# Performance work log

Measured on AMD Instinct MI355X. Metric: run time of the kernel, lower is better.

The kernel has to match this reference:

```python
import jax, jax.numpy as jnp
import numpy as np

jax.config.update("jax_enable_x64", True)

L_MAX = 9  # matches init_kwargs; K = (L_MAX+1)**2 = 100 modes
SQRT_2_OVER_PI = float(np.sqrt(2.0 / np.pi))


def _l_array(l_max):
    # l repeated 2l+1 times (one entry per (l, m) mode), as float like torch.Tensor
    ls = np.concatenate([np.full(2 * i + 1, i) for i in range(l_max + 1)])
    return jnp.asarray(ls, dtype=jnp.float64)


def _bessel_up(r, k, l_arr, l_max):
    x = r.astype(jnp.float64)[..., None] * k.astype(jnp.float64)  # [N, K]
    j0 = jnp.sin(x) / x
    y = jnp.where(l_arr == 0, j0, 0.0)
    j1 = j0 / x - jnp.cos(x) / x
    y = jnp.where(l_arr == 1, j1, y)
    for i in range(1, l_max):  # small static loop over l (l_max-1 iters)
        j2 = (2 * i + 1) / x * j1 - j0
        y = jnp.where(l_arr == i + 1, j2, y)
        j0, j1 = j1, j2
    y = jnp.where(jnp.abs(x) < 1e-30, 0.0, y)
    y = y * SQRT_2_OVER_PI * k.astype(jnp.float64)
    return y.astype(jnp.float32)


def _bessel_down(r, k, l_arr, l_max):
    x = r.astype(jnp.float64)[..., None] * k.astype(jnp.float64)  # [N, K]
    y = jnp.zeros_like(x)
    lstart = l_max + int(np.sqrt(10 * l_max))
    j2 = jnp.zeros_like(x)
    j1 = jnp.ones_like(x)
    j0 = j1
    for i in range(lstart, 0, -1):  # small static downward recurrence
        j0 = (2 * i + 1) / x * j1 - j2
        if i - 1 < l_max + 1:
            y = jnp.where(l_arr == (i - 1), j0, y)
        j2, j1 = j1, j0
    true_j0 = jnp.sinc(x / jnp.pi)  # = sin(x)/x, matches torch.sinc(r/pi)
    y = y / j0 * true_j0
    small = x < 1e-20
    y = jnp.where(small & (l_arr > 0), 0.0, y)
    y = jnp.where(small & (l_arr == 0), 1.0, y)
    y = y * SQRT_2_OVER_PI * k.astype(jnp.float64)
    return y.astype(jnp.float32)


def setup_inputs() -> dict:
    key = jax.random.key(0)
    k1, k2 = jax.random.split(key)
    N = 262144
    K = (L_MAX + 1) ** 2  # 100
    r = jax.random.uniform(k1, (N,), dtype=jnp.float32, minval=0.1, maxval=20.0)
    k = jax.random.uniform(k2, (K,), dtype=jnp.float32, minval=0.5, maxval=5.0)
    return {"r": r, "k": k}


def reference(r, k):
    l_arr = _l_array(L_MAX)
    up = _bessel_up(r, k, l_arr, L_MAX)    # [N, K] f32
    dn = _bessel_down(r, k, l_arr, L_MAX)  # [N, K] f32
    x32 = r[..., None] * k                 # f32, like the torch forward
    return jnp.where(x32 < l_arr.astype(jnp.float32), dn, up)
```

## Files before the change

kernel.cpp:

```cpp
#include <hip/hip_runtime.h>
#include <math.h>


static constexpr int KMODES  = 100;
static constexpr int NTILE   = 64;
static constexpr int LSTRIDE = 102;
static constexpr double PI_D   = 3.14159265358979323846;
static constexpr double BETA_D = 1.0 / (2.0 * PI_D);
static constexpr double S2PI_D = 0.79788456080286535588;

__device__ __forceinline__ float rcpf(float x) { return __builtin_amdgcn_rcpf(x); }
__device__ __forceinline__ float sin_rev(float a) { float r; asm("v_sin_f32 %0, %1" : "=v"(r) : "v"(a)); return r; }
__device__ __forceinline__ float cos_rev(float a) { float r; asm("v_cos_f32 %0, %1" : "=v"(r) : "v"(a)); return r; }

template<int L> struct ZC;
template<> struct ZC<2>{ static constexpr double sg[2]={3,-1};                              static constexpr double gm[1]={-3}; };
template<> struct ZC<3>{ static constexpr double sg[2]={15,-6};                             static constexpr double gm[2]={-15,1}; };
template<> struct ZC<4>{ static constexpr double sg[3]={105,-45,1};                         static constexpr double gm[2]={-105,10}; };
template<> struct ZC<5>{ static constexpr double sg[3]={945,-420,15};                       static constexpr double gm[3]={-945,105,-1}; };
template<> struct ZC<6>{ static constexpr double sg[4]={10395,-4725,210,-1};                static constexpr double gm[3]={-10395,1260,-21}; };
template<> struct ZC<7>{ static constexpr double sg[4]={135135,-62370,3150,-28};            static constexpr double gm[4]={-135135,17325,-378,1}; };
template<> struct ZC<8>{ static constexpr double sg[5]={2027025,-945945,51975,-630,1};      static constexpr double gm[4]={-2027025,270270,-6930,36}; };
template<> struct ZC<9>{ static constexpr double sg[5]={34459425,-16216200,945945,-13860,45}; static constexpr double gm[5]={-34459425,4729725,-135135,990,-1}; };

template<int L> struct WC {
  static constexpr int NS = L / 2 + 1, NG = (L + 1) / 2;
  float sg[NS], gm[NG], xc;
  constexpr WC() : sg{}, gm{}, xc(0.f) {
    constexpr double XT[10] = {0,0,0.088,0.29,0.61,1.01,1.48,2.00,2.55,3.14};
    for (int i = 0; i < NS; ++i) {
      int deg = NS - 1 - i, e = (L & 1) ? (2*deg + 2) : (2*deg + 1);
      double s = S2PI_D; for (int t = 0; t < e; ++t) s *= BETA_D;
      sg[i] = (float)(s * ZC<L>::sg[i]);
    }
    for (int i = 0; i < NG; ++i) {
      int deg = NG - 1 - i, e = (L & 1) ? (2*deg + 1) : (2*deg + 2);
      double s = S2PI_D; for (int t = 0; t < e; ++t) s *= BETA_D;
      gm[i] = (float)(s * ZC<L>::gm[i]);
    }
    xc = (float)(XT[L] * BETA_D);
  }
};

template<int N>
__device__ __forceinline__ float polyH(float y, const float (&a)[N]) {
  float h = a[0];
#pragma unroll
  for (int i = 1; i < N; ++i) h = fmaf(h, y, a[i]);
  return h;
}

template<int L>
__device__ __forceinline__ void do_l(float rv, const float2* __restrict__ ktab,
                                     float* ldsrow) {
#pragma unroll
  for (int m = 0; m < 2 * L + 1; ++m) {
    const int KK = L * L + m;
    float2 kp = ktab[KK];
    float arg = rv * kp.x;
    float res;
    if constexpr (L == 0) {
      float w = rcpf(arg);
      float s = sin_rev(arg);
      res = (s * (float)(S2PI_D * BETA_D)) * (kp.y * w);
    } else if constexpr (L == 1) {
      float w = rcpf(arg);
      float s = sin_rev(arg), c = cos_rev(arg);
      float t = c * (float)(S2PI_D * BETA_D);
      float inner = fmaf(s * w, (float)(S2PI_D * BETA_D * BETA_D), -t);
      res = (kp.y * w) * inner;
    } else {
      constexpr WC<L> wc{};
      float argc = fmaxf(arg, wc.xc);
      float w = rcpf(argc);
      float s = sin_rev(argc), c = cos_rev(argc);
      float y = w * w;
      float sgv = polyH(y, wc.sg);
      float gmv = polyH(y, wc.gm);
      float inner;
      if constexpr (L & 1) inner = fmaf(s * w, sgv, c * gmv);
      else                 inner = fmaf(c * w, gmv, s * sgv);
      res = (kp.y * w) * inner;
    }
    ldsrow[KK] = res;
  }
}

__global__ __launch_bounds__(256) void sbf_kernel(const float* __restrict__ r,
                                                  const float* __restrict__ kvec,
                                                  float* __restrict__ out) {
  __shared__ float2 ktab[KMODES];
  __shared__ float lds[NTILE * LSTRIDE];
  const int tid = threadIdx.x;
  const int w = tid >> 6, lane = tid & 63;
  const int n0 = blockIdx.x * NTILE;
  if (tid < KMODES) {
    float kv = kvec[tid];
    ktab[tid] = make_float2(kv * (float)BETA_D, kv);
  }
  float rv = r[n0 + lane];
  float* ldsrow = &lds[lane * LSTRIDE];
  __syncthreads();
  if (w == 0)      { do_l<9>(rv, ktab, ldsrow); do_l<2>(rv, ktab, ldsrow); }
  else if (w == 1) { do_l<8>(rv, ktab, ldsrow); do_l<3>(rv, ktab, ldsrow); }
  else if (w == 2) { do_l<7>(rv, ktab, ldsrow); do_l<4>(rv, ktab, ldsrow); do_l<0>(rv, ktab, ldsrow); }
  else             { do_l<6>(rv, ktab, ldsrow); do_l<5>(rv, ktab, ldsrow); do_l<1>(rv, ktab, ldsrow); }
  __syncthreads();
  unsigned e0 = (unsigned)tid * 4u;
  int row = (int)(e0 / 100u);
  int col = (int)e0 - row * 100;
  int wi  = row * LSTRIDE + col;
  float* gout = out + (size_t)n0 * KMODES + e0;
#pragma unroll
  for (int it = 0; it < 6; ++it) {
    float2 lo = *reinterpret_cast<const float2*>(&lds[wi]);
    float2 hi = *reinterpret_cast<const float2*>(&lds[wi + 2]);
    *reinterpret_cast<float4*>(gout + it * 1024) = make_float4(lo.x, lo.y, hi.x, hi.y);
    col += 24; wi += 1044;
    if (col >= 100) { col -= 100; wi += 2; }
  }
  if (tid < 64) {
    float2 lo = *reinterpret_cast<const float2*>(&lds[wi]);
    float2 hi = *reinterpret_cast<const float2*>(&lds[wi + 2]);
    *reinterpret_cast<float4*>(gout + 6 * 1024) = make_float4(lo.x, lo.y, hi.x, hi.y);
  }
}

extern "C" void kernel_launch(void* const* d_in, const int* in_sizes, int n_in,
                              void* d_out, int out_size, void* d_ws, size_t ws_size,
                              hipStream_t stream) {
  const float* r = (const float*)d_in[0];
  const float* k = (const float*)d_in[1];
  float* out = (float*)d_out;
  int N = in_sizes[0];
  int blocks = N / NTILE;
  sbf_kernel<<<blocks, 256, 0, stream>>>(r, k, out);
}
```

Baseline: 24.78 us.

## Process four tiles per block with double-buffered LDS and interleaved output flushing

Each block now handles four 64-point tiles and writes them into two alternating LDS buffers. The global stores of the previous tile are spread through the compute loop of the next tile via a Flusher that runs after every third mode. The aim is to overlap output writes with transcendental compute and to drop the per-block ktab setup, since k is read directly from global (scalar) memory and r is pre-scaled by 1/(2π). The unpadded LDS stride may add bank conflicts on the per-lane row writes. There are also 4x fewer blocks, which lowers occupancy and parallelism across the GPU.

```diff
diff --git a/kernel.cpp b/kernel.cpp
--- a/kernel.cpp
+++ b/kernel.cpp
@@ -2,9 +2,10 @@
 #include <math.h>
 
 
-static constexpr int KMODES  = 100;
-static constexpr int NTILE   = 64;
-static constexpr int LSTRIDE = 102;
+static constexpr int KMODES = 100;
+static constexpr int NTILE  = 64;
+static constexpr int TPB    = 4;
+static constexpr int TILE_ELEMS = NTILE * KMODES;
 static constexpr double PI_D   = 3.14159265358979323846;
 static constexpr double BETA_D = 1.0 / (2.0 * PI_D);
 static constexpr double S2PI_D = 0.79788456080286535588;
@@ -50,25 +51,42 @@
   return h;
 }
 
+struct Flusher {
+  const float* src; float* dst; int it; int tid;
+  __device__ __forceinline__ void step() {
+    if (src != nullptr && it < 7) {
+      int e = it * 1024 + tid * 4;
+      if (it < 6 || tid < 64) {
+        float4 v = *reinterpret_cast<const float4*>(src + e);
+        *reinterpret_cast<float4*>(dst + e) = v;
+      }
+      ++it;
+      __builtin_amdgcn_sched_barrier(0);
+    }
+  }
+  __device__ __forceinline__ void finish() {
+    if (src != nullptr) { while (it < 7) step(); }
+  }
+};
+
 template<int L>
-__device__ __forceinline__ void do_l(float rv, const float2* __restrict__ ktab,
-                                     float* ldsrow) {
+__device__ __forceinline__ void do_l(float rvb, const float* __restrict__ kvec,
+                                     float* ldsrow, Flusher& fl) {
 #pragma unroll
   for (int m = 0; m < 2 * L + 1; ++m) {
     const int KK = L * L + m;
-    float2 kp = ktab[KK];
-    float arg = rv * kp.x;
+    float kv = kvec[KK];
+    float arg = rvb * kv;
     float res;
     if constexpr (L == 0) {
       float w = rcpf(arg);
-      float s = sin_rev(arg);
-      res = (s * (float)(S2PI_D * BETA_D)) * (kp.y * w);
+      res = (sin_rev(arg) * (float)(S2PI_D * BETA_D)) * (kv * w);
     } else if constexpr (L == 1) {
       float w = rcpf(arg);
       float s = sin_rev(arg), c = cos_rev(arg);
-      float t = c * (float)(S2PI_D * BETA_D);
-      float inner = fmaf(s * w, (float)(S2PI_D * BETA_D * BETA_D), -t);
-      res = (kp.y * w) * inner;
+      float inner = fmaf(s * w, (float)(S2PI_D * BETA_D * BETA_D),
+                         -(c * (float)(S2PI_D * BETA_D)));
+      res = (kv * w) * inner;
     } else {
       constexpr WC<L> wc{};
       float argc = fmaxf(arg, wc.xc);
@@ -80,50 +98,42 @@
       float inner;
       if constexpr (L & 1) inner = fmaf(s * w, sgv, c * gmv);
       else                 inner = fmaf(c * w, gmv, s * sgv);
-      res = (kp.y * w) * inner;
+      res = (kv * w) * inner;
     }
     ldsrow[KK] = res;
+    if ((m % 3) == 2) fl.step();
   }
 }
 
 __global__ __launch_bounds__(256) void sbf_kernel(const float* __restrict__ r,
                                                   const float* __restrict__ kvec,
                                                   float* __restrict__ out) {
-  __shared__ float2 ktab[KMODES];
-  __shared__ float lds[NTILE * LSTRIDE];
+  __shared__ float buf[2][TILE_ELEMS];
   const int tid = threadIdx.x;
   const int w = tid >> 6, lane = tid & 63;
-  const int n0 = blockIdx.x * NTILE;
-  if (tid < KMODES) {
-    float kv = kvec[tid];
-    ktab[tid] = make_float2(kv * (float)BETA_D, kv);
+  const int tile0 = blockIdx.x * TPB;
+
+  float rvb[TPB];
+#pragma unroll
+  for (int t = 0; t < TPB; ++t)
+    rvb[t] = r[(tile0 + t) * NTILE + lane] * (float)BETA_D;
+
+  Flusher fl{nullptr, nullptr, 7, tid};
+#pragma unroll
+  for (int t = 0; t < TPB; ++t) {
+    float* ldsrow = &buf[t & 1][lane * KMODES];
+    if (w == 0)      { do_l<9>(rvb[t], kvec, ldsrow, fl); do_l<2>(rvb[t], kvec, ldsrow, fl); }
+    else if (w == 1) { do_l<8>(rvb[t], kvec, ldsrow, fl); do_l<3>(rvb[t], kvec, ldsrow, fl); }
+    else if (w == 2) { do_l<7>(rvb[t], kvec, ldsrow, fl); do_l<4>(rvb[t], kvec, ldsrow, fl); do_l<0>(rvb[t], kvec, ldsrow, fl); }
+    else             { do_l<6>(rvb[t], kvec, ldsrow, fl); do_l<5>(rvb[t], kvec, ldsrow, fl); do_l<1>(rvb[t], kvec, ldsrow, fl); }
+    fl.finish();
+    asm volatile("s_waitcnt lgkmcnt(0)" ::: "memory");
+    __builtin_amdgcn_s_barrier();
+    fl.src = &buf[t & 1][0];
+    fl.dst = out + (size_t)(tile0 + t) * TILE_ELEMS;
+    fl.it = 0;
   }
-  float rv = r[n0 + lane];
-  float* ldsrow = &lds[lane * LSTRIDE];
-  __syncthreads();
-  if (w == 0)      { do_l<9>(rv, ktab, ldsrow); do_l<2>(rv, ktab, ldsrow); }
-  else if (w == 1) { do_l<8>(rv, ktab, ldsrow); do_l<3>(rv, ktab, ldsrow); }
-  else if (w == 2) { do_l<7>(rv, ktab, ldsrow); do_l<4>(rv, ktab, ldsrow); do_l<0>(rv, ktab, ldsrow); }
-  else             { do_l<6>(rv, ktab, ldsrow); do_l<5>(rv, ktab, ldsrow); do_l<1>(rv, ktab, ldsrow); }
-  __syncthreads();
-  unsigned e0 = (unsigned)tid * 4u;
-  int row = (int)(e0 / 100u);
-  int col = (int)e0 - row * 100;
-  int wi  = row * LSTRIDE + col;
-  float* gout = out + (size_t)n0 * KMODES + e0;
-#pragma unroll
-  for (int it = 0; it < 6; ++it) {
-    float2 lo = *reinterpret_cast<const float2*>(&lds[wi]);
-    float2 hi = *reinterpret_cast<const float2*>(&lds[wi + 2]);
-    *reinterpret_cast<float4*>(gout + it * 1024) = make_float4(lo.x, lo.y, hi.x, hi.y);
-    col += 24; wi += 1044;
-    if (col >= 100) { col -= 100; wi += 2; }
-  }
-  if (tid < 64) {
-    float2 lo = *reinterpret_cast<const float2*>(&lds[wi]);
-    float2 hi = *reinterpret_cast<const float2*>(&lds[wi + 2]);
-    *reinterpret_cast<float4*>(gout + 6 * 1024) = make_float4(lo.x, lo.y, hi.x, hi.y);
-  }
+  fl.finish();
 }
 
 extern "C" void kernel_launch(void* const* d_in, const int* in_sizes, int n_in,
@@ -133,6 +143,6 @@
   const float* k = (const float*)d_in[1];
   float* out = (float*)d_out;
   int N = in_sizes[0];
-  int blocks = N / NTILE;
+  int blocks = N / NTILE / TPB;
   sbf_kernel<<<blocks, 256, 0, stream>>>(r, k, out);
 }
```

Result: slower. 26.18 us (+5.6%).
